# Kernel optimization log

Measured on AMD Instinct MI355X. Metric: run time of the kernel, lower is better.

## Reference

```python
import jax, jax.numpy as jnp
import numpy as np

B, NB, C, FEAT = 2, 512, 80, 1024
FIRST_N = 128
NMS_FC = 128
POS_EMB = 64
GROUPS = 16
ATT_D = (1024, 1024, 128)
NUM_THRESH = 3
BBOX_W = (10.0, 10.0, 5.0, 5.0)
SCALE_CLAMP = float(np.log(1000.0 / 16.0))


def setup_inputs() -> dict:
    key = jax.random.key(0)
    ks = jax.random.split(key, 24)
    roi_feat = jax.random.normal(ks[0], (B * NB, FEAT), jnp.float32)
    scores = jax.random.normal(ks[1], (B * NB, C + 1), jnp.float32)
    proposal_deltas = jax.random.normal(ks[2], (B * NB, C * 4), jnp.float32) * 0.5
    xy = jax.random.uniform(ks[3], (B * NB, 2), jnp.float32) * 800.0
    wh = jax.random.uniform(ks[4], (B * NB, 2), jnp.float32) * 100.0 + 1.0
    proposal_boxes = jnp.concatenate([xy, xy + wh], axis=1)

    def lin(k, fin, fout, std=0.01):
        return jax.random.normal(k, (fin, fout), jnp.float32) * std

    return {
        'roi_feat': roi_feat,
        'scores': scores,
        'proposal_deltas': proposal_deltas,
        'proposal_boxes': proposal_boxes,
        'roi_w': lin(ks[5], FEAT, NMS_FC), 'roi_b': jnp.zeros((NMS_FC,), jnp.float32),
        'rank_w': lin(ks[6], FEAT, NMS_FC), 'rank_b': jnp.zeros((NMS_FC,), jnp.float32),
        'logit_w': lin(ks[7], NMS_FC, NUM_THRESH), 'logit_b': jnp.full((NUM_THRESH,), -3.0, jnp.float32),
        'pos_w': lin(ks[8], POS_EMB, GROUPS), 'pos_b': jnp.zeros((GROUPS,), jnp.float32),
        'q_w': lin(ks[9], NMS_FC, ATT_D[0]), 'q_b': jnp.zeros((ATT_D[0],), jnp.float32),
        'k_w': lin(ks[10], NMS_FC, ATT_D[1]), 'k_b': jnp.zeros((ATT_D[1],), jnp.float32),
        'out_w': jax.random.normal(ks[11], (GROUPS, NMS_FC, ATT_D[2] // GROUPS), jnp.float32) * 0.01,
        'out_b': jnp.zeros((ATT_D[2],), jnp.float32),
        'num_boxes': NB,
    }


def _rank_embedding():
    # sinusoidal rank embedding, dim FEAT
    fr = jnp.arange(FEAT // 2, dtype=jnp.float32)
    dim_mat = jnp.power(1000.0, (2.0 / FEAT) * fr)
    div = jnp.arange(FIRST_N, dtype=jnp.float32)[:, None] / dim_mat[None, :]
    return jnp.concatenate([jnp.sin(div), jnp.cos(div)], axis=1)  # (FIRST_N, FEAT)


def _pos_embed(boxes):
    # boxes: (FIRST_N, C, 4) -> (C, N, N, POS_EMB)
    b = jnp.transpose(boxes, (1, 0, 2))  # (C, N, 4)
    x1, y1, x2, y2 = b[..., 0], b[..., 1], b[..., 2], b[..., 3]
    w = x2 - x1 + 1.0
    h = y2 - y1 + 1.0
    cx = 0.5 * (x1 + x2)
    cy = 0.5 * (y1 + y2)
    dx = jnp.log(jnp.maximum(jnp.abs((cx[:, :, None] - cx[:, None, :]) / w[:, :, None]), 1e-3))
    dy = jnp.log(jnp.maximum(jnp.abs((cy[:, :, None] - cy[:, None, :]) / h[:, :, None]), 1e-3))
    dw = jnp.log(w[:, :, None] / w[:, None, :])
    dh = jnp.log(h[:, :, None] / h[:, None, :])
    pm = jnp.stack([dx, dy, dw, dh], axis=-1)  # (C, N, N, 4)
    fr = jnp.arange(POS_EMB // 8, dtype=jnp.float32)
    dim_mat = jnp.power(1000.0, (8.0 / POS_EMB) * fr)
    dv = (pm * 100.0)[..., None] / dim_mat  # (C, N, N, 4, POS_EMB//8)
    e = jnp.concatenate([jnp.sin(dv), jnp.cos(dv)], axis=-1)  # (C, N, N, 4, POS_EMB//4)
    return e.reshape(pm.shape[:3] + (POS_EMB,))


def reference(roi_feat, scores, proposal_deltas, proposal_boxes,
              roi_w, roi_b, rank_w, rank_b, logit_w, logit_b,
              pos_w, pos_b, q_w, q_b, k_w, k_b, out_w, out_b, num_boxes):
    deltas = jax.lax.stop_gradient(proposal_deltas)  # detached in original
    pboxes = jax.lax.stop_gradient(proposal_boxes)
    batch = deltas.shape[0] // num_boxes

    # ---- Box2BoxTransform.apply_deltas ----
    widths = pboxes[:, 2] - pboxes[:, 0]
    heights = pboxes[:, 3] - pboxes[:, 1]
    ctr_x = pboxes[:, 0] + 0.5 * widths
    ctr_y = pboxes[:, 1] + 0.5 * heights
    wx, wy, ww, wh = BBOX_W
    d = deltas.reshape(-1, C, 4)
    dx = d[..., 0] / wx
    dy = d[..., 1] / wy
    dw = jnp.minimum(d[..., 2] / ww, SCALE_CLAMP)
    dh = jnp.minimum(d[..., 3] / wh, SCALE_CLAMP)
    pcx = dx * widths[:, None] + ctr_x[:, None]
    pcy = dy * heights[:, None] + ctr_y[:, None]
    pw = jnp.exp(dw) * widths[:, None]
    ph = jnp.exp(dh) * heights[:, None]
    refined = jnp.stack([pcx - 0.5 * pw, pcy - 0.5 * ph, pcx + 0.5 * pw, pcy + 0.5 * ph], axis=-1)
    refined = refined.reshape(batch, num_boxes, C, 4)

    # ---- softmax + per-class descending sort, keep first_n ----
    sc = scores.reshape(batch, num_boxes, C + 1)
    probs = jax.nn.softmax(sc[..., :C], axis=1)
    rank_idxs = jnp.argsort(-probs, axis=1)[:, :FIRST_N, :]  # (B, FIRST_N, C)
    sorted_score = jnp.take_along_axis(probs, rank_idxs, axis=1)  # (B, FIRST_N, C)
    sorted_boxes = jax.vmap(lambda bx, i: jnp.take_along_axis(bx, i[..., None], axis=0))(refined, rank_idxs)  # (B, FIRST_N, C, 4)

    # ---- rank + roi embeddings ----
    rank_feat = _rank_embedding() @ rank_w + rank_b  # (FIRST_N, NMS_FC)
    roi_emb = (roi_feat @ roi_w + roi_b).reshape(batch, num_boxes, NMS_FC)
    sorted_roi = jax.vmap(lambda e, i: e[i])(roi_emb, rank_idxs)  # (B, FIRST_N, C, NMS_FC)
    emb_feat = sorted_roi + rank_feat[None, :, None, :]

    dq = ATT_D[0] // GROUPS
    dk = ATT_D[1] // GROUPS

    def attend(feat, boxes):
        # feat: (FIRST_N, C, NMS_FC), boxes: (FIRST_N, C, 4)
        pe = _pos_embed(boxes)  # (C, N, N, POS_EMB)
        aff_w = jax.nn.relu(pe @ pos_w + pos_b)  # (C, N, N, G)
        aff_w = jnp.transpose(aff_w, (0, 3, 1, 2))  # (C, G, N, N)
        f = jnp.transpose(feat, (1, 0, 2))  # (C, N, NMS_FC)
        q = (f @ q_w + q_b).reshape(C, FIRST_N, GROUPS, dq).transpose(0, 2, 1, 3)
        k = (f @ k_w + k_b).reshape(C, FIRST_N, GROUPS, dk).transpose(0, 2, 1, 3)
        aff = jnp.einsum('cgnd,cgmd->cgnm', q, k) / jnp.sqrt(jnp.float32(dk))
        sm = jax.nn.softmax(jnp.log(jnp.maximum(aff_w, 1e-6)) + aff, axis=-1)
        ov = jnp.einsum('cgnm,cmd->cgnd', sm, f)  # (C, G, N, NMS_FC)
        lin = jnp.einsum('cgnd,gde->cnge', ov, out_w).reshape(C, FIRST_N, ATT_D[2]) + out_b
        return jnp.transpose(lin, (1, 0, 2))  # (N, C, ATT_D[2])

    att = jax.vmap(attend)(emb_feat, sorted_boxes)
    all_feat = jax.nn.relu(emb_feat + att)
    logit = all_feat @ logit_w + logit_b  # (B, FIRST_N, C, NUM_THRESH)
    nms_multi_score = jax.nn.sigmoid(logit) * sorted_score[..., None]
    return nms_multi_score
```

## Files before the change

### kernel.cpp

```cpp
#include <hip/hip_runtime.h>
#include <math.h>

#define B_    2
#define NB_   512
#define C_    80
#define FEAT_ 1024
#define FN_   128
#define FC_   128
#define PE_   64
#define G_    16
#define DQ_   64
#define EO_   8
#define NT_   3
#define SCALE_CLAMP_ 4.135166556742356f

typedef __attribute__((ext_vector_type(8))) short bf16x8;
typedef __attribute__((ext_vector_type(4))) float f32x4;

#define O_ROIP    ((size_t)0)
#define O_RANKP   (O_ROIP + (size_t)2*B_*NB_*FC_)
#define O_RANKIDX (O_RANKP + (size_t)2*FN_*FC_)
#define O_SSCORE  (O_RANKIDX + (size_t)B_*FN_*C_)
#define O_SBOX    (O_SSCORE + (size_t)B_*FN_*C_)
#define O_EMB     (O_SBOX + (size_t)B_*FN_*C_*4)
#define O_ATT     (O_EMB + (size_t)B_*FN_*C_*FC_)
#define O_LW      (O_ATT + (size_t)B_*FN_*C_*FC_)

__device__ __forceinline__ float bf2f(unsigned short u) {
    return __uint_as_float(((unsigned int)u) << 16);
}
__device__ __forceinline__ unsigned short f2bf(float f) {
    unsigned int x = __float_as_uint(f);
    unsigned int r = (x + 0x7fff + ((x >> 16) & 1)) >> 16;
    return (unsigned short)r;
}
__device__ __forceinline__ unsigned short f2h(float x) {
    _Float16 h = (_Float16)x;
    return __builtin_bit_cast(unsigned short, h);
}
__device__ __forceinline__ float h2f(unsigned short u) {
    _Float16 h = __builtin_bit_cast(_Float16, u);
    return (float)h;
}

#define ADDR128(row, gr)  ((row)*128 + ((((gr) ^ ((row)&7))) << 4))

__global__ __launch_bounds__(256) void k_embed(const float* __restrict__ roi_feat,
                                               const float* __restrict__ roi_w,
                                               const float* __restrict__ roi_b,
                                               const float* __restrict__ rank_w,
                                               const float* __restrict__ rank_b,
                                               float* __restrict__ roiP,
                                               float* __restrict__ rankP)
{
    const int bid = blockIdx.x;
    const int kh  = bid & 1;
    const int rt  = bid >> 1;
    const bool isRank = rt >= 64;
    const int row0 = (isRank ? rt - 64 : rt) * 16;
    const int t = threadIdx.x;
    const int w = t >> 6, lane = t & 63, lr = lane & 15, lh = lane >> 4;
    const int col0 = w * 32;
    const float* W = isRank ? rank_w : roi_w;
    const float* bias = isRank ? rank_b : roi_b;

    const int arow = row0 + lr;
    f32x4 acc0 = {0,0,0,0}, acc1 = {0,0,0,0};

    #pragma unroll 4
    for (int ks = 0; ks < 16; ++ks) {
        const int kb = kh*512 + ks*32 + lh*8;
        bf16x8 af;
        if (!isRank) {
            float4 a0 = *(const float4*)(roi_feat + (size_t)arow*FEAT_ + kb);
            float4 a1 = *(const float4*)(roi_feat + (size_t)arow*FEAT_ + kb + 4);
            af[0] = (short)f2bf(a0.x); af[1] = (short)f2bf(a0.y);
            af[2] = (short)f2bf(a0.z); af[3] = (short)f2bf(a0.w);
            af[4] = (short)f2bf(a1.x); af[5] = (short)f2bf(a1.y);
            af[6] = (short)f2bf(a1.z); af[7] = (short)f2bf(a1.w);
        } else {
            #pragma unroll
            for (int j = 0; j < 8; ++j) {
                int k = kb + j;
                int kk = k & 511;
                float inv = exp2f(-(float)kk * 0.0194644226f);
                float arg = (float)arow * inv;
                float v = (k < 512) ? __sinf(arg) : __cosf(arg);
                af[j] = (short)f2bf(v);
            }
        }
        bf16x8 bf0, bf1;
        #pragma unroll
        for (int j = 0; j < 8; ++j) {
            const float* wr = W + (size_t)(kb + j)*FC_ + col0 + lr;
            bf0[j] = (short)f2bf(wr[0]);
            bf1[j] = (short)f2bf(wr[16]);
        }
        acc0 = __builtin_amdgcn_mfma_f32_16x16x32_bf16(af, bf0, acc0, 0, 0, 0);
        acc1 = __builtin_amdgcn_mfma_f32_16x16x32_bf16(af, bf1, acc1, 0, 0, 0);
    }
    float* dst = isRank ? (rankP + (size_t)kh*FN_*FC_) : (roiP + (size_t)kh*(B_*NB_)*FC_);
    #pragma unroll
    for (int tile = 0; tile < 2; ++tile) {
        f32x4 a = tile ? acc1 : acc0;
        int col = col0 + tile*16 + lr;
        float bv = (kh == 0) ? bias[col] : 0.0f;
        #pragma unroll
        for (int reg = 0; reg < 4; ++reg) {
            int rr = row0 + lh*4 + reg;
            dst[(size_t)rr*FC_ + col] = a[reg] + bv;
        }
    }
}

__global__ __launch_bounds__(512) void k_topk(const float* __restrict__ scores,
                                              int* __restrict__ rank_idx,
                                              float* __restrict__ sorted_score)
{
    int b = blockIdx.x / C_, c = blockIdx.x % C_;
    __shared__ float p[NB_];
    __shared__ float red[NB_];
    int i = threadIdx.x;
    float s = scores[(size_t)(b*NB_ + i)*(C_+1) + c];
    red[i] = s; __syncthreads();
    for (int o = 256; o > 0; o >>= 1) { if (i < o) red[i] = fmaxf(red[i], red[i+o]); __syncthreads(); }
    float mx = red[0]; __syncthreads();
    float e = expf(s - mx);
    red[i] = e; __syncthreads();
    for (int o = 256; o > 0; o >>= 1) { if (i < o) red[i] += red[i+o]; __syncthreads(); }
    float sum = red[0]; __syncthreads();
    float pi = e / sum;
    p[i] = pi; __syncthreads();
    int rank = 0;
    for (int j4 = 0; j4 < NB_/4; ++j4) {
        float4 pj = *(const float4*)&p[j4*4];
        int j = j4*4;
        rank += (pj.x > pi) || (pj.x == pi && (j+0) < i);
        rank += (pj.y > pi) || (pj.y == pi && (j+1) < i);
        rank += (pj.z > pi) || (pj.z == pi && (j+2) < i);
        rank += (pj.w > pi) || (pj.w == pi && (j+3) < i);
    }
    if (rank < FN_) {
        rank_idx[(size_t)(b*FN_ + rank)*C_ + c] = i;
        sorted_score[(size_t)(b*FN_ + rank)*C_ + c] = pi;
    }
}

__global__ __launch_bounds__(256) void k_gather(const int* __restrict__ rank_idx,
                                                const float* __restrict__ roiP,
                                                const float* __restrict__ rankP,
                                                const float* __restrict__ pdeltas,
                                                const float* __restrict__ pboxes,
                                                float* __restrict__ emb_feat,
                                                float* __restrict__ sorted_boxes)
{
    const int t = threadIdx.x;
    const int item = blockIdx.x*8 + (t >> 5);
    const int l = t & 31;
    const int c = item % C_;
    const int bn = item / C_;
    const int n = bn & (FN_-1);
    const int b = bn >> 7;
    const int idx = rank_idx[item];
    const int row = b*NB_ + idx;
    float4 e0 = *(const float4*)(roiP + (size_t)row*FC_ + l*4);
    float4 e1 = *(const float4*)(roiP + (size_t)(B_*NB_ + row)*FC_ + l*4);
    float4 r0 = *(const float4*)(rankP + (size_t)n*FC_ + l*4);
    float4 r1 = *(const float4*)(rankP + (size_t)(FN_ + n)*FC_ + l*4);
    *(float4*)(emb_feat + (size_t)item*FC_ + l*4) =
        make_float4(e0.x+e1.x+r0.x+r1.x, e0.y+e1.y+r0.y+r1.y,
                    e0.z+e1.z+r0.z+r1.z, e0.w+e1.w+r0.w+r1.w);
    if (l == 0) {
        float x1 = pboxes[row*4+0], y1 = pboxes[row*4+1], x2 = pboxes[row*4+2], y2 = pboxes[row*4+3];
        float w = x2 - x1, h = y2 - y1;
        float cx = x1 + 0.5f*w, cy = y1 + 0.5f*h;
        const float* dl = pdeltas + (size_t)row*(C_*4) + c*4;
        float dx = dl[0]/10.0f, dy = dl[1]/10.0f;
        float dw = fminf(dl[2]/5.0f, SCALE_CLAMP_);
        float dh = fminf(dl[3]/5.0f, SCALE_CLAMP_);
        float pcx = dx*w + cx, pcy = dy*h + cy;
        float pw = expf(dw)*w, ph = expf(dh)*h;
        float* ob = sorted_boxes + (size_t)item*4;
        ob[0] = pcx - 0.5f*pw; ob[1] = pcy - 0.5f*ph;
        ob[2] = pcx + 0.5f*pw; ob[3] = pcy + 0.5f*ph;
    }
}

__global__ __launch_bounds__(256) void k_pos2(const float* __restrict__ sorted_boxes,
                                              const float* __restrict__ pos_w,
                                              const float* __restrict__ pos_b,
                                              unsigned short* __restrict__ lw)
{
    const int n2   = blockIdx.x & 63;
    const int rest = blockIdx.x >> 6;
    const int cl   = rest % C_;
    const int b    = rest / C_;
    const int n0   = n2 * 2;
    const int t    = threadIdx.x;

    __shared__ float geomL[FN_][6];
    __shared__ unsigned short featL[256*PE_];
    __shared__ unsigned short poswL[G_*PE_];
    __shared__ float pbL[G_];
    __shared__ float sdimL[8];

    if (t < FN_) {
        const float* bx = sorted_boxes + (((size_t)(b*FN_ + t))*C_ + cl)*4;
        float x1 = bx[0], y1 = bx[1], x2 = bx[2], y2 = bx[3];
        float w = x2 - x1 + 1.0f;
        float h = y2 - y1 + 1.0f;
        geomL[t][0] = 0.5f*(x1+x2);
        geomL[t][1] = 0.5f*(y1+y2);
        geomL[t][2] = w;
        geomL[t][3] = h;
        geomL[t][4] = __logf(w);
        geomL[t][5] = __logf(h);
    } else {
        int id = t - 128;
        int g  = id >> 3;
        int gr = id & 7;
        unsigned short u[8];
        #pragma unroll
        for (int j = 0; j < 8; ++j) u[j] = f2bf(pos_w[(gr*8 + j)*G_ + g]);
        *(uint4*)((char*)poswL + ADDR128(g, gr)) =
            make_uint4((unsigned)u[0] | ((unsigned)u[1] << 16),
                       (unsigned)u[2] | ((unsigned)u[3] << 16),
                       (unsigned)u[4] | ((unsigned)u[5] << 16),
                       (unsigned)u[6] | ((unsigned)u[7] << 16));
    }
    if (t < G_) pbL[t] = pos_b[t];
    if (t >= 16 && t < 24) sdimL[t-16] = 1.0f / powf(1000.0f, 0.125f*(float)(t-16));
    __syncthreads();

    {
        const int nl = t >> 7;
        const int m  = t & 127;
        const int n  = n0 + nl;
        float pm[4];
        {
            float cxn = geomL[n][0], cyn = geomL[n][1];
            float rwn = 1.0f/geomL[n][2], rhn = 1.0f/geomL[n][3];
            pm[0] = __logf(fmaxf(fabsf((cxn - geomL[m][0]) * rwn), 1e-3f)) * 100.0f;
            pm[1] = __logf(fmaxf(fabsf((cyn - geomL[m][1]) * rhn), 1e-3f)) * 100.0f;
            pm[2] = (geomL[n][4] - geomL[m][4]) * 100.0f;
            pm[3] = (geomL[n][5] - geomL[m][5]) * 100.0f;
        }
        char* base = (char*)featL;
        #pragma unroll
        for (int f = 0; f < 4; ++f) {
            float s[8], c[8];
            #pragma unroll
            for (int r = 0; r < 8; ++r) {
                __sincosf(pm[f] * sdimL[r], &s[r], &c[r]);
            }
            unsigned short us[8], uc[8];
            #pragma unroll
            for (int r = 0; r < 8; ++r) { us[r] = f2bf(s[r]); uc[r] = f2bf(c[r]); }
            *(uint4*)(base + ADDR128(t, 2*f)) =
                make_uint4((unsigned)us[0] | ((unsigned)us[1] << 16),
                           (unsigned)us[2] | ((unsigned)us[3] << 16),
                           (unsigned)us[4] | ((unsigned)us[5] << 16),
                           (unsigned)us[6] | ((unsigned)us[7] << 16));
            *(uint4*)(base + ADDR128(t, 2*f + 1)) =
                make_uint4((unsigned)uc[0] | ((unsigned)uc[1] << 16),
                           (unsigned)uc[2] | ((unsigned)uc[3] << 16),
                           (unsigned)uc[4] | ((unsigned)uc[5] << 16),
                           (unsigned)uc[6] | ((unsigned)uc[7] << 16));
        }
    }
    __syncthreads();

    {
        const int wave = t >> 6, lane = t & 63;
        const int lr = lane & 15, lh = lane >> 4;
        const float pbg = pbL[lr];
        #pragma unroll
        for (int ti = 0; ti < 4; ++ti) {
            const int t16 = wave*4 + ti;
            f32x4 acc = {0,0,0,0};
            #pragma unroll
            for (int ks = 0; ks < 2; ++ks) {
                bf16x8 a  = *(const bf16x8*)((char*)featL + ADDR128(t16*16 + lr, ks*4 + lh));
                bf16x8 bb = *(const bf16x8*)((char*)poswL + ADDR128(lr, ks*4 + lh));
                acc = __builtin_amdgcn_mfma_f32_16x16x32_bf16(a, bb, acc, 0, 0, 0);
            }
            const int g = lr;
            #pragma unroll
            for (int reg = 0; reg < 4; ++reg) {
                int p = t16*16 + lh*4 + reg;
                int n = n0 + (p >> 7);
                int m = p & 127;
                float w = fmaxf(fmaxf(acc[reg] + pbg, 0.0f), 1e-6f);
                lw[(((size_t)(b*C_ + cl)*FN_ + n)*G_ + g)*FN_ + m] = f2h(__logf(w));
            }
        }
    }
}

#define FT_OFF   0
#define QL_OFF   34816
#define KL_OFF   51200
#define VT_OFF   67584
#define BIAS_OFF 71680
#define SMEM_SZ  72192

__global__ __launch_bounds__(1024, 8) void k_attn(const float* __restrict__ emb_feat,
                                               const float* __restrict__ q_w, const float* __restrict__ q_b,
                                               const float* __restrict__ k_w, const float* __restrict__ k_b,
                                               const float* __restrict__ out_w, const float* __restrict__ out_b,
                                               const unsigned short* __restrict__ lw,
                                               float* __restrict__ att)
{
    const int g    = blockIdx.x & 15;
    const int rest = blockIdx.x >> 4;
    const int cl   = rest % C_;
    const int b    = rest / C_;
    const int c    = cl;
    const int t  = threadIdx.x;
    const int wave = t >> 6;
    const int lane = t & 63;
    const int lr = lane & 15;
    const int lh = lane >> 4;

    __shared__ char smem[SMEM_SZ];
    float* biasL = (float*)(smem + BIAS_OFF);

    for (int s = 0; s < 4; ++s) {
        int fi = t + s*1024;
        int n  = fi >> 5;
        int d4 = (fi & 31) << 2;
        float4 v = *(const float4*)(emb_feat + ((size_t)(b*FN_ + n)*C_ + c)*FC_ + d4);
        char* dst = smem + FT_OFF + n*272 + (fi & 31)*8;
        *(uint2*)dst = make_uint2((unsigned)f2bf(v.x) | ((unsigned)f2bf(v.y) << 16),
                                  (unsigned)f2bf(v.z) | ((unsigned)f2bf(v.w) << 16));
    }
    if (t >= 512 && t < 768) {
        int i = t - 512;
        *(uint2*)(smem + VT_OFF + 8*256 + i*8) = make_uint2(0u, 0u);
    }
    if (t >= 128 && t < 256) {
        int r = t - 128;
        biasL[r] = (r < 64) ? q_b[g*DQ_ + r] : k_b[g*DQ_ + (r-64)];
    }
    __syncthreads();

    {
        const int rb = (wave >> 2) * 32;
        const int nb = (wave & 3) * 32;
        const float* wsrc = (rb < 64) ? q_w : k_w;
        const int col0 = g*DQ_ + (rb & 63) + lr;
        f32x4 acc00 = {0,0,0,0}, acc01 = {0,0,0,0}, acc10 = {0,0,0,0}, acc11 = {0,0,0,0};
        f32x4 accV  = {0,0,0,0};
        #pragma unroll
        for (int ks = 0; ks < 4; ++ks) {
            const int k0 = ks*32 + lh*8;
            bf16x8 a0, a1;
            #pragma unroll
            for (int j = 0; j < 8; ++j) {
                const float* kp = wsrc + (size_t)(k0 + j)*1024;
                a0[j] = (short)f2bf(kp[col0]);
                a1[j] = (short)f2bf(kp[col0 + 16]);
            }
            const int fo = ks*64 + lh*16;
            bf16x8 b0 = *(const bf16x8*)(smem + FT_OFF + (nb + lr)*272 + fo);
            bf16x8 b1 = *(const bf16x8*)(smem + FT_OFF + (nb + 16 + lr)*272 + fo);
            acc00 = __builtin_amdgcn_mfma_f32_16x16x32_bf16(a0, b0, acc00, 0, 0, 0);
            acc01 = __builtin_amdgcn_mfma_f32_16x16x32_bf16(a0, b1, acc01, 0, 0, 0);
            acc10 = __builtin_amdgcn_mfma_f32_16x16x32_bf16(a1, b0, acc10, 0, 0, 0);
            acc11 = __builtin_amdgcn_mfma_f32_16x16x32_bf16(a1, b1, acc11, 0, 0, 0);
            if (wave < 8) {
                bf16x8 av;
                #pragma unroll
                for (int j = 0; j < 8; ++j)
                    av[j] = (lr < 8) ? (short)f2bf(out_w[(size_t)g*1024 + (size_t)(k0 + j)*8 + lr]) : (short)0;
                bf16x8 bv = *(const bf16x8*)(smem + FT_OFF + (wave*16 + lr)*272 + fo);
                accV = __builtin_amdgcn_mfma_f32_16x16x32_bf16(av, bv, accV, 0, 0, 0);
            }
        }
        #pragma unroll
        for (int ti = 0; ti < 2; ++ti) {
            #pragma unroll
            for (int tj = 0; tj < 2; ++tj) {
                f32x4 a = (ti == 0) ? (tj == 0 ? acc00 : acc01) : (tj == 0 ? acc10 : acc11);
                int r0 = rb + ti*16 + lh*4;
                int n  = nb + tj*16 + lr;
                float v0 = a[0] + biasL[r0+0];
                float v1 = a[1] + biasL[r0+1];
                float v2 = a[2] + biasL[r0+2];
                float v3 = a[3] + biasL[r0+3];
                int dq0 = r0 & 63;
                int off = (r0 < 64 ? QL_OFF : KL_OFF);
                char* dst = smem + off + ADDR128(n, dq0 >> 3) + ((dq0 >> 2) & 1)*8;
                *(uint2*)dst = make_uint2((unsigned)f2bf(v0) | ((unsigned)f2bf(v1) << 16),
                                          (unsigned)f2bf(v2) | ((unsigned)f2bf(v3) << 16));
            }
        }
        if (wave < 8 && lh < 2) {
            int m = wave*16 + lr;
            #pragma unroll
            for (int reg = 0; reg < 4; ++reg) {
                int e = lh*4 + reg;
                char* dst = smem + VT_OFF + (e)*256 + ((((m >> 3) ^ e)) << 4) + (m & 7)*2;
                *(unsigned short*)dst = f2bf(accV[reg]);
            }
        }
    }
    __syncthreads();

    {
        const int nb = (wave >> 2) * 32;
        const int mb = (wave & 3) * 32;
        f32x4 acc00 = {0,0,0,0}, acc01 = {0,0,0,0}, acc10 = {0,0,0,0}, acc11 = {0,0,0,0};
        #pragma unroll
        for (int ks = 0; ks < 2; ++ks) {
            int soff = ((ks*4 + lh) ^ (lr & 7)) << 4;
            bf16x8 a0 = *(const bf16x8*)(smem + QL_OFF + (nb + lr)*128 + soff);
            bf16x8 a1 = *(const bf16x8*)(smem + QL_OFF + (nb + 16 + lr)*128 + soff);
            bf16x8 b0 = *(const bf16x8*)(smem + KL_OFF + (mb + lr)*128 + soff);
            bf16x8 b1 = *(const bf16x8*)(smem + KL_OFF + (mb + 16 + lr)*128 + soff);
            acc00 = __builtin_amdgcn_mfma_f32_16x16x32_bf16(a0, b0, acc00, 0, 0, 0);
            acc01 = __builtin_amdgcn_mfma_f32_16x16x32_bf16(a0, b1, acc01, 0, 0, 0);
            acc10 = __builtin_amdgcn_mfma_f32_16x16x32_bf16(a1, b0, acc10, 0, 0, 0);
            acc11 = __builtin_amdgcn_mfma_f32_16x16x32_bf16(a1, b1, acc11, 0, 0, 0);
        }
        #pragma unroll
        for (int ti = 0; ti < 2; ++ti) {
            #pragma unroll
            for (int tj = 0; tj < 2; ++tj) {
                f32x4 a = (ti == 0) ? (tj == 0 ? acc00 : acc01) : (tj == 0 ? acc10 : acc11);
                int n0 = nb + ti*16 + lh*4;
                int m  = mb + tj*16 + lr;
                #pragma unroll
                for (int reg = 0; reg < 4; ++reg)
                    *(unsigned short*)(smem + FT_OFF + (n0 + reg)*272 + 2*m) = f2h(a[reg]);
            }
        }
    }
    __syncthreads();

    {
        const int row = t >> 3;
        const int lp  = t & 7;
        const int m0  = lp * 16;
        const unsigned short* lwrow = lw + ((((size_t)(b*C_ + cl))*FN_ + row)*G_ + g)*FN_ + m0;
        uint4 gl0 = *(const uint4*)(lwrow);
        uint4 gl1 = *(const uint4*)(lwrow + 8);
        char* abase = smem + FT_OFF + row*272 + lp*32;
        uint4 af0 = *(const uint4*)abase;
        uint4 af1 = *(const uint4*)(abase + 16);
        const unsigned short* ah0 = (const unsigned short*)&af0;
        const unsigned short* ah1 = (const unsigned short*)&af1;
        const unsigned short* lp0 = (const unsigned short*)&gl0;
        const unsigned short* lp1 = (const unsigned short*)&gl1;
        float v[16];
        float mx = -INFINITY;
        #pragma unroll
        for (int j = 0; j < 8; ++j) {
            float val = h2f(ah0[j])*0.125f + h2f(lp0[j]);
            v[j] = val; mx = fmaxf(mx, val);
        }
        #pragma unroll
        for (int j = 0; j < 8; ++j) {
            float val = h2f(ah1[j])*0.125f + h2f(lp1[j]);
            v[8+j] = val; mx = fmaxf(mx, val);
        }
        #pragma unroll
        for (int s = 1; s < 8; s <<= 1) mx = fmaxf(mx, __shfl_xor(mx, s, 8));
        float sum = 0.f;
        #pragma unroll
        for (int j = 0; j < 16; ++j) { v[j] = __expf(v[j] - mx); sum += v[j]; }
        #pragma unroll
        for (int s = 1; s < 8; s <<= 1) sum += __shfl_xor(sum, s, 8);
        float rs = 1.0f / sum;
        unsigned short u[16];
        #pragma unroll
        for (int j = 0; j < 16; ++j) u[j] = f2bf(v[j] * rs);
        *(uint4*)abase = make_uint4((unsigned)u[0] | ((unsigned)u[1] << 16),
                                    (unsigned)u[2] | ((unsigned)u[3] << 16),
                                    (unsigned)u[4] | ((unsigned)u[5] << 16),
                                    (unsigned)u[6] | ((unsigned)u[7] << 16));
        *(uint4*)(abase + 16) = make_uint4((unsigned)u[8]  | ((unsigned)u[9]  << 16),
                                           (unsigned)u[10] | ((unsigned)u[11] << 16),
                                           (unsigned)u[12] | ((unsigned)u[13] << 16),
                                           (unsigned)u[14] | ((unsigned)u[15] << 16));
    }
    __syncthreads();

    if (wave < 8) {
        const int tb = wave * 16;
        f32x4 acc = {0,0,0,0};
        #pragma unroll
        for (int ks = 0; ks < 4; ++ks) {
            const int fo = ks*64 + lh*16;
            int soff = ((ks*4 + lh) ^ lr) << 4;
            bf16x8 a = *(const bf16x8*)(smem + FT_OFF + (tb + lr)*272 + fo);
            bf16x8 bv = *(const bf16x8*)(smem + VT_OFF + lr*256 + soff);
            acc = __builtin_amdgcn_mfma_f32_16x16x32_bf16(a, bv, acc, 0, 0, 0);
        }
        if (lr < 8) {
            float ob = out_b[g*EO_ + lr];
            #pragma unroll
            for (int reg = 0; reg < 4; ++reg) {
                int n = tb + lh*4 + reg;
                att[((size_t)(b*FN_ + n)*C_ + c)*FC_ + g*EO_ + lr] = acc[reg] + ob;
            }
        }
    }
}

__global__ __launch_bounds__(256) void k_final(const float* __restrict__ emb_feat,
                                               const float* __restrict__ att,
                                               const float* __restrict__ logit_w,
                                               const float* __restrict__ logit_b,
                                               const float* __restrict__ sorted_score,
                                               float* __restrict__ out)
{
    __shared__ float lwL[FC_*NT_ + NT_];
    const int t = threadIdx.x;
    for (int i = t; i < FC_*NT_ + NT_; i += 256)
        lwL[i] = (i < FC_*NT_) ? logit_w[i] : logit_b[i - FC_*NT_];
    __syncthreads();
    const int item = blockIdx.x*8 + (t >> 5);
    const int l = t & 31;
    const int d0 = l*4;
    float4 ev = *(const float4*)(emb_feat + (size_t)item*FC_ + d0);
    float4 av = *(const float4*)(att + (size_t)item*FC_ + d0);
    float a0 = fmaxf(ev.x + av.x, 0.f);
    float a1 = fmaxf(ev.y + av.y, 0.f);
    float a2 = fmaxf(ev.z + av.z, 0.f);
    float a3 = fmaxf(ev.w + av.w, 0.f);
    float s0 = a0*lwL[(d0+0)*NT_+0] + a1*lwL[(d0+1)*NT_+0] + a2*lwL[(d0+2)*NT_+0] + a3*lwL[(d0+3)*NT_+0];
    float s1 = a0*lwL[(d0+0)*NT_+1] + a1*lwL[(d0+1)*NT_+1] + a2*lwL[(d0+2)*NT_+1] + a3*lwL[(d0+3)*NT_+1];
    float s2 = a0*lwL[(d0+0)*NT_+2] + a1*lwL[(d0+1)*NT_+2] + a2*lwL[(d0+2)*NT_+2] + a3*lwL[(d0+3)*NT_+2];
    #pragma unroll
    for (int s = 1; s < 32; s <<= 1) {
        s0 += __shfl_xor(s0, s, 32);
        s1 += __shfl_xor(s1, s, 32);
        s2 += __shfl_xor(s2, s, 32);
    }
    if (l < NT_) {
        float lg = (l == 0) ? s0 : (l == 1) ? s1 : s2;
        lg += lwL[FC_*NT_ + l];
        float sg = 1.f / (1.f + expf(-lg));
        out[(size_t)item*NT_ + l] = sg * sorted_score[item];
    }
}

extern "C" void kernel_launch(void* const* d_in, const int* in_sizes, int n_in,
                              void* d_out, int out_size, void* d_ws, size_t ws_size,
                              hipStream_t stream) {
    (void)in_sizes; (void)n_in; (void)out_size; (void)ws_size;
    const float* roi_feat = (const float*)d_in[0];
    const float* scores   = (const float*)d_in[1];
    const float* pdeltas  = (const float*)d_in[2];
    const float* pboxes   = (const float*)d_in[3];
    const float* roi_w    = (const float*)d_in[4];
    const float* roi_b    = (const float*)d_in[5];
    const float* rank_w   = (const float*)d_in[6];
    const float* rank_b   = (const float*)d_in[7];
    const float* logit_w  = (const float*)d_in[8];
    const float* logit_b  = (const float*)d_in[9];
    const float* pos_w    = (const float*)d_in[10];
    const float* pos_b    = (const float*)d_in[11];
    const float* q_w      = (const float*)d_in[12];
    const float* q_b      = (const float*)d_in[13];
    const float* k_w      = (const float*)d_in[14];
    const float* k_b      = (const float*)d_in[15];
    const float* out_w    = (const float*)d_in[16];
    const float* out_b    = (const float*)d_in[17];
    float* ws = (float*)d_ws;

    float* roiP         = ws + O_ROIP;
    float* rankP        = ws + O_RANKP;
    int*   rank_idx     = (int*)(ws + O_RANKIDX);
    float* sorted_score = ws + O_SSCORE;
    float* sorted_boxes = ws + O_SBOX;
    float* emb_feat     = ws + O_EMB;
    float* att          = ws + O_ATT;
    unsigned short* lwb = (unsigned short*)(ws + O_LW);

    k_embed<<<dim3(144), dim3(256), 0, stream>>>(roi_feat, roi_w, roi_b, rank_w, rank_b,
                                                 roiP, rankP);
    k_topk<<<dim3(B_*C_), dim3(512), 0, stream>>>(scores, rank_idx, sorted_score);
    k_gather<<<dim3(B_*FN_*C_/8), dim3(256), 0, stream>>>(rank_idx, roiP, rankP,
                                                          pdeltas, pboxes, emb_feat, sorted_boxes);
    k_pos2<<<dim3(B_*C_*64), dim3(256), 0, stream>>>(sorted_boxes, pos_w, pos_b, lwb);
    k_attn<<<dim3(B_*C_*G_), dim3(1024), 0, stream>>>(emb_feat, q_w, q_b, k_w, k_b,
                                                      out_w, out_b, lwb, att);
    k_final<<<dim3(B_*FN_*C_/8), dim3(256), 0, stream>>>(emb_feat, att, logit_w, logit_b,
                                                         sorted_score, d_out ? (float*)d_out : nullptr);
}
```

Before: 188.3 us.

## Prepack q/k/out weights to bf16 and emit bf16 embeddings for attention

Adds a k_prep kernel that transposes q_w, k_w and out_w into a per-group bf16 layout once per call. k_gather now also writes a bf16 copy of emb_feat. k_attn then loads weights and features with 16-byte vector loads instead of doing strided scalar fp32 reads and conversions in each of the 2560 blocks. The cost is one extra small launch, an extra bf16 write in gather, and more workspace.

```diff
diff --git a/kernel.cpp b/kernel.cpp
--- a/kernel.cpp
+++ b/kernel.cpp
@@ -25,6 +25,8 @@
 #define O_EMB     (O_SBOX + (size_t)B_*FN_*C_*4)
 #define O_ATT     (O_EMB + (size_t)B_*FN_*C_*FC_)
 #define O_LW      (O_ATT + (size_t)B_*FN_*C_*FC_)
+#define O_WT      (O_LW + (size_t)B_*C_*FN_*G_*FN_/2)
+#define O_EMBB    (O_WT + (size_t)16*144*128/2)
 
 __device__ __forceinline__ float bf2f(unsigned short u) {
     return __uint_as_float(((unsigned int)u) << 16);
@@ -44,6 +46,40 @@
 }
 
 #define ADDR128(row, gr)  ((row)*128 + ((((gr) ^ ((row)&7))) << 4))
+
+__global__ __launch_bounds__(256) void k_prep(const float* __restrict__ q_w,
+                                              const float* __restrict__ k_w,
+                                              const float* __restrict__ out_w,
+                                              unsigned short* __restrict__ wt)
+{
+    const int g = blockIdx.x;
+    const int t = threadIdx.x;
+    for (int idx = t; idx < 144*16; idx += 256) {
+        const int row = idx >> 4;
+        const int kc  = (idx & 15) * 8;
+        unsigned short u[8];
+        if (row < 64) {
+            #pragma unroll
+            for (int j = 0; j < 8; ++j) u[j] = f2bf(q_w[(size_t)(kc + j)*1024 + g*DQ_ + row]);
+        } else if (row < 128) {
+            const int r = row - 64;
+            #pragma unroll
+            for (int j = 0; j < 8; ++j) u[j] = f2bf(k_w[(size_t)(kc + j)*1024 + g*DQ_ + r]);
+        } else if (row < 136) {
+            const int e = row - 128;
+            #pragma unroll
+            for (int j = 0; j < 8; ++j) u[j] = f2bf(out_w[(size_t)g*FC_*EO_ + (size_t)(kc + j)*EO_ + e]);
+        } else {
+            #pragma unroll
+            for (int j = 0; j < 8; ++j) u[j] = 0;
+        }
+        *(uint4*)(wt + (size_t)g*144*128 + row*128 + kc) =
+            make_uint4((unsigned)u[0] | ((unsigned)u[1] << 16),
+                       (unsigned)u[2] | ((unsigned)u[3] << 16),
+                       (unsigned)u[4] | ((unsigned)u[5] << 16),
+                       (unsigned)u[6] | ((unsigned)u[7] << 16));
+    }
+}
 
 __global__ __launch_bounds__(256) void k_embed(const float* __restrict__ roi_feat,
                                                const float* __restrict__ roi_w,
@@ -152,6 +188,7 @@
                                                 const float* __restrict__ pdeltas,
                                                 const float* __restrict__ pboxes,
                                                 float* __restrict__ emb_feat,
+                                                unsigned short* __restrict__ embB,
                                                 float* __restrict__ sorted_boxes)
 {
     const int t = threadIdx.x;
@@ -167,9 +204,12 @@
     float4 e1 = *(const float4*)(roiP + (size_t)(B_*NB_ + row)*FC_ + l*4);
     float4 r0 = *(const float4*)(rankP + (size_t)n*FC_ + l*4);
     float4 r1 = *(const float4*)(rankP + (size_t)(FN_ + n)*FC_ + l*4);
-    *(float4*)(emb_feat + (size_t)item*FC_ + l*4) =
-        make_float4(e0.x+e1.x+r0.x+r1.x, e0.y+e1.y+r0.y+r1.y,
-                    e0.z+e1.z+r0.z+r1.z, e0.w+e1.w+r0.w+r1.w);
+    float4 sm = make_float4(e0.x+e1.x+r0.x+r1.x, e0.y+e1.y+r0.y+r1.y,
+                            e0.z+e1.z+r0.z+r1.z, e0.w+e1.w+r0.w+r1.w);
+    *(float4*)(emb_feat + (size_t)item*FC_ + l*4) = sm;
+    *(uint2*)(embB + (size_t)item*FC_ + l*4) =
+        make_uint2((unsigned)f2bf(sm.x) | ((unsigned)f2bf(sm.y) << 16),
+                   (unsigned)f2bf(sm.z) | ((unsigned)f2bf(sm.w) << 16));
     if (l == 0) {
         float x1 = pboxes[row*4+0], y1 = pboxes[row*4+1], x2 = pboxes[row*4+2], y2 = pboxes[row*4+3];
         float w = x2 - x1, h = y2 - y1;
@@ -304,10 +344,11 @@
 #define BIAS_OFF 71680
 #define SMEM_SZ  72192
 
-__global__ __launch_bounds__(1024, 8) void k_attn(const float* __restrict__ emb_feat,
-                                               const float* __restrict__ q_w, const float* __restrict__ q_b,
-                                               const float* __restrict__ k_w, const float* __restrict__ k_b,
-                                               const float* __restrict__ out_w, const float* __restrict__ out_b,
+__global__ __launch_bounds__(1024, 8) void k_attn(const unsigned short* __restrict__ embB,
+                                               const unsigned short* __restrict__ wt,
+                                               const float* __restrict__ q_b,
+                                               const float* __restrict__ k_b,
+                                               const float* __restrict__ out_b,
                                                const unsigned short* __restrict__ lw,
                                                float* __restrict__ att)
 {
@@ -325,14 +366,16 @@
     __shared__ char smem[SMEM_SZ];
     float* biasL = (float*)(smem + BIAS_OFF);
 
-    for (int s = 0; s < 4; ++s) {
-        int fi = t + s*1024;
-        int n  = fi >> 5;
-        int d4 = (fi & 31) << 2;
-        float4 v = *(const float4*)(emb_feat + ((size_t)(b*FN_ + n)*C_ + c)*FC_ + d4);
-        char* dst = smem + FT_OFF + n*272 + (fi & 31)*8;
-        *(uint2*)dst = make_uint2((unsigned)f2bf(v.x) | ((unsigned)f2bf(v.y) << 16),
-                                  (unsigned)f2bf(v.z) | ((unsigned)f2bf(v.w) << 16));
+    {
+        const char* src = (const char*)embB + ((size_t)(b*FN_)*C_ + c)*FC_*2;
+        #pragma unroll
+        for (int s = 0; s < 2; ++s) {
+            int fi = t + s*1024;
+            int n  = fi >> 4;
+            int o16 = (fi & 15) * 16;
+            uint4 v = *(const uint4*)(src + (size_t)n*C_*FC_*2 + o16);
+            *(uint4*)(smem + FT_OFF + n*272 + o16) = v;
+        }
     }
     if (t >= 512 && t < 768) {
         int i = t - 512;
@@ -347,21 +390,14 @@
     {
         const int rb = (wave >> 2) * 32;
         const int nb = (wave & 3) * 32;
-        const float* wsrc = (rb < 64) ? q_w : k_w;
-        const int col0 = g*DQ_ + (rb & 63) + lr;
+        const char* wtg = (const char*)wt + (size_t)g*144*256;
         f32x4 acc00 = {0,0,0,0}, acc01 = {0,0,0,0}, acc10 = {0,0,0,0}, acc11 = {0,0,0,0};
         f32x4 accV  = {0,0,0,0};
         #pragma unroll
         for (int ks = 0; ks < 4; ++ks) {
-            const int k0 = ks*32 + lh*8;
-            bf16x8 a0, a1;
-            #pragma unroll
-            for (int j = 0; j < 8; ++j) {
-                const float* kp = wsrc + (size_t)(k0 + j)*1024;
-                a0[j] = (short)f2bf(kp[col0]);
-                a1[j] = (short)f2bf(kp[col0 + 16]);
-            }
             const int fo = ks*64 + lh*16;
+            bf16x8 a0 = *(const bf16x8*)(wtg + (rb + lr)*256 + fo);
+            bf16x8 a1 = *(const bf16x8*)(wtg + (rb + 16 + lr)*256 + fo);
             bf16x8 b0 = *(const bf16x8*)(smem + FT_OFF + (nb + lr)*272 + fo);
             bf16x8 b1 = *(const bf16x8*)(smem + FT_OFF + (nb + 16 + lr)*272 + fo);
             acc00 = __builtin_amdgcn_mfma_f32_16x16x32_bf16(a0, b0, acc00, 0, 0, 0);
@@ -369,10 +405,7 @@
             acc10 = __builtin_amdgcn_mfma_f32_16x16x32_bf16(a1, b0, acc10, 0, 0, 0);
             acc11 = __builtin_amdgcn_mfma_f32_16x16x32_bf16(a1, b1, acc11, 0, 0, 0);
             if (wave < 8) {
-                bf16x8 av;
-                #pragma unroll
-                for (int j = 0; j < 8; ++j)
-                    av[j] = (lr < 8) ? (short)f2bf(out_w[(size_t)g*1024 + (size_t)(k0 + j)*8 + lr]) : (short)0;
+                bf16x8 av = *(const bf16x8*)(wtg + (128 + lr)*256 + fo);
                 bf16x8 bv = *(const bf16x8*)(smem + FT_OFF + (wave*16 + lr)*272 + fo);
                 accV = __builtin_amdgcn_mfma_f32_16x16x32_bf16(av, bv, accV, 0, 0, 0);
             }
@@ -578,15 +611,17 @@
     float* emb_feat     = ws + O_EMB;
     float* att          = ws + O_ATT;
     unsigned short* lwb = (unsigned short*)(ws + O_LW);
-
+    unsigned short* wtb = (unsigned short*)(ws + O_WT);
+    unsigned short* embB = (unsigned short*)(ws + O_EMBB);
+
+    k_prep<<<dim3(G_), dim3(256), 0, stream>>>(q_w, k_w, out_w, wtb);
     k_embed<<<dim3(144), dim3(256), 0, stream>>>(roi_feat, roi_w, roi_b, rank_w, rank_b,
                                                  roiP, rankP);
     k_topk<<<dim3(B_*C_), dim3(512), 0, stream>>>(scores, rank_idx, sorted_score);
     k_gather<<<dim3(B_*FN_*C_/8), dim3(256), 0, stream>>>(rank_idx, roiP, rankP,
-                                                          pdeltas, pboxes, emb_feat, sorted_boxes);
+                                                          pdeltas, pboxes, emb_feat, embB, sorted_boxes);
     k_pos2<<<dim3(B_*C_*64), dim3(256), 0, stream>>>(sorted_boxes, pos_w, pos_b, lwb);
-    k_attn<<<dim3(B_*C_*G_), dim3(1024), 0, stream>>>(emb_feat, q_w, q_b, k_w, k_b,
-                                                      out_w, out_b, lwb, att);
+    k_attn<<<dim3(B_*C_*G_), dim3(1024), 0, stream>>>(embB, wtb, q_b, k_b, out_b, lwb, att);
     k_final<<<dim3(B_*FN_*C_/8), dim3(256), 0, stream>>>(emb_feat, att, logit_w, logit_b,
                                                          sorted_score, d_out ? (float*)d_out : nullptr);
 }
```

New measurement: 195.7 us. 1.04x slower.
